# Kernel tuning notes

Measured on AMD Instinct MI355X. Metric: run time of the kernel, lower is better.

The kernel has to match this reference:

```python
import jax, jax.numpy as jnp
import numpy as np

S, L, T, E, H = 512, 5, 20, 768, 64


def setup_inputs() -> dict:
    key = jax.random.key(0)
    ks = jax.random.split(key, 32)

    def p(k, shape, scale=0.05):
        return jax.random.normal(k, shape, dtype=jnp.float32) * scale

    return {
        "text_input": jax.random.normal(ks[0], (S, L, T, E), dtype=jnp.float32),
        "time_inputs": jax.random.uniform(ks[1], (S, L, T), dtype=jnp.float32),
        # TimeLSTM per-stock params (gate order f, i, o, c_tmp)
        "Wall": p(ks[2], (S, H, 4 * H)), "bWall": p(ks[3], (S, 4 * H)),
        "Uall": p(ks[4], (S, E, 4 * H)), "bUall": p(ks[5], (S, 4 * H)),
        "Wd": p(ks[6], (S, H, H)), "bWd": p(ks[7], (S, H)),
        # shared text/day Attention per stock
        "W1": p(ks[8], (S, H, H)), "b1": p(ks[9], (S, H)),
        "W2": p(ks[10], (S, H, H)), "b2": p(ks[11], (S, H)),
        "V": p(ks[12], (S, H, 1)), "bV": p(ks[13], (S, 1)),
        # day nn.LSTM per stock (gate order i, f, g, o)
        "Wih": p(ks[14], (S, H, 4 * H)), "Whh": p(ks[15], (S, H, 4 * H)),
        "bih": p(ks[16], (S, 4 * H)), "bhh": p(ks[17], (S, 4 * H)),
        # shared output head
        "lin_w": p(ks[18], (H, 1)), "lin_b": p(ks[19], (1,)),
        "no_stocks": S,
    }


def _forward(text_input, time_inputs, Wall, bWall, Uall, bUall, Wd, bWd,
             W1, b1, W2, b2, V, bV, Wih, Whh, bih, bhh, lin_w, lin_b, no_stocks):
    def per_stock(x, ts, Wall, bWall, Uall, bUall, Wd, bWd,
                  W1, b1, W2, b2, V, bV, Wih, Whh, bih, bhh):
        # x: [L, T, E], ts: [L, T] -- lookback days are an inner batch for the TimeLSTM
        u = jnp.einsum('lte,eg->ltg', x, Uall) + bUall  # [L, T, 4H]

        def step(carry, inp):
            h, c = carry                 # [L, H]
            u_t, ts_t = inp              # [L, 4H], [L]
            c_s1 = jnp.tanh(c @ Wd + bWd)
            c_adj = (c - c_s1) + c_s1 * ts_t[:, None]
            gates = h @ Wall + bWall + u_t
            f, i, o, c_tmp = jnp.split(gates, 4, axis=1)
            f = jax.nn.sigmoid(f)
            i = jax.nn.sigmoid(i)
            o = jax.nn.sigmoid(o)
            c_tmp = jax.nn.sigmoid(c_tmp)  # sigmoid (not tanh), faithful to source
            c_new = f * c_adj + i * c_tmp
            h_new = o * jnp.tanh(c_new)
            return (h_new, c_new), o     # module collects the o gate as 'outputs'

        init = (jnp.zeros((L, H), x.dtype), jnp.zeros((L, H), x.dtype))
        (h_fin, _), o_seq = jax.lax.scan(step, init, (u.transpose(1, 0, 2), ts.T))
        full = o_seq.transpose(1, 0, 2)  # [L, T, H]

        # text attention: score = V(tanh(W1(last) + W2(full))), softmax over T
        score = jnp.tanh((h_fin @ W1 + b1)[:, None, :] + full @ W2 + b2) @ V + bV  # [L, T, 1]
        aw = jax.nn.softmax(score, axis=1)
        text_vec = jnp.sum(aw * full, axis=1)  # [L, H]

        # day nn.LSTM: input (1, L, H) seq-first => one cell step with batch=L, zero state
        h0 = jnp.zeros((L, H), x.dtype)
        g = text_vec @ Wih + bih + h0 @ Whh + bhh
        gi, gf, gg, go = jnp.split(g, 4, axis=1)
        c_d = jax.nn.sigmoid(gi) * jnp.tanh(gg)  # f * c0 = 0
        h_d = jax.nn.sigmoid(go) * jnp.tanh(c_d)  # [L, H]; output == h_n here

        # day attention reuses the SAME text_attention weights; full == last == h_d
        s2 = jnp.tanh(h_d @ W1 + b1 + h_d @ W2 + b2) @ V + bV  # [L, 1]
        aw2 = jax.nn.softmax(s2, axis=0)
        return jnp.sum(aw2 * h_d, axis=0)  # [H]

    ft_vec = jax.vmap(per_stock)(text_input, time_inputs, Wall, bWall, Uall, bUall,
                                 Wd, bWd, W1, b1, W2, b2, V, bV,
                                 Wih, Whh, bih, bhh)  # [S, H]
    return jax.nn.leaky_relu(ft_vec @ lin_w + lin_b, negative_slope=0.01)  # [S, 1]


def reference(text_input, time_inputs, Wall, bWall, Uall, bUall, Wd, bWd,
              W1, b1, W2, b2, V, bV, Wih, Whh, bih, bhh, lin_w, lin_b, no_stocks):
    return _forward(text_input, time_inputs, Wall, bWall, Uall, bUall, Wd, bWd,
                    W1, b1, W2, b2, V, bV, Wih, Whh, bih, bhh, lin_w, lin_b, no_stocks)
```

## Files before the change

kernel.cpp:

```cpp
#include <hip/hip_runtime.h>
#include <cstddef>

#define NS 512
#define NL 5
#define NT 20
#define NE 768
#define NH 64
#define NG 256

__device__ __forceinline__ float sigf(float x) { return 1.0f / (1.0f + expf(-x)); }
__device__ __forceinline__ float bcast(float v, int k) {
    return __int_as_float(__builtin_amdgcn_readlane(__float_as_int(v), k));
}

typedef __fp16 h16x2 __attribute__((ext_vector_type(2)));
typedef _Float16 f16x8 __attribute__((ext_vector_type(8)));
typedef __attribute__((ext_vector_type(4))) float f32x4;

union PkU { h16x2 h; unsigned u; };

__device__ __forceinline__ void split_pk(float a, float b, unsigned& hi, unsigned& lo) {
    PkU H, L;
    H.h = __builtin_amdgcn_cvt_pkrtz(a, b);
    float ra = a - (float)H.h[0];
    float rb = b - (float)H.h[1];
    L.h = __builtin_amdgcn_cvt_pkrtz(ra, rb);
    hi = H.u; lo = L.u;
}

__device__ __forceinline__ void stage8(const float v[8], unsigned short* base, unsigned off) {
    uint4 ph, pl;
    split_pk(v[0], v[1], ph.x, pl.x);
    split_pk(v[2], v[3], ph.y, pl.y);
    split_pk(v[4], v[5], ph.z, pl.z);
    split_pk(v[6], v[7], ph.w, pl.w);
    *(uint4*)&base[off]       = ph;
    *(uint4*)&base[off + 512] = pl;
}

__global__ __launch_bounds__(512, 4) void k_gemm_u(
    const float* __restrict__ x, const float* __restrict__ U,
    const float* __restrict__ bU, float* __restrict__ u)
{
    __shared__ unsigned short Af[8 * 2 * 512];
    __shared__ unsigned short Bf[8 * 2 * 512];
    const int bid = blockIdx.x;
    const int s = bid >> 1, half = bid & 1;
    const int tid = threadIdx.x;
    const int wave = tid >> 6, lane = tid & 63;
    const int wm = wave & 1, wn = wave >> 1;
    const float* xg = x + (size_t)s * (NL * NT * NE);
    const float* Ug = U + (size_t)s * (NE * NG) + half * 128;

    f32x4 acc[4][2] = {};

    const int arow = tid >> 2, ab = tid & 3;
    const unsigned a_off = ((unsigned)(arow >> 4) * 2) * 512 + ((arow & 15) + 16 * ab) * 8;
    const int bcol = tid & 127, bkq = tid >> 7;
    const unsigned b_off = ((unsigned)(bcol >> 4) * 2) * 512 + ((bcol & 15) + 16 * bkq) * 8;

    float av[8], bv[8];
    {
        const float* pa = xg + (size_t)arow * NE + ab * 8;
        if (arow < 100) {
            float4 q0 = *(const float4*)pa, q1 = *(const float4*)(pa + 4);
            av[0]=q0.x; av[1]=q0.y; av[2]=q0.z; av[3]=q0.w;
            av[4]=q1.x; av[5]=q1.y; av[6]=q1.z; av[7]=q1.w;
        } else {
            #pragma unroll
            for (int j = 0; j < 8; ++j) av[j] = 0.0f;
        }
        #pragma unroll
        for (int j = 0; j < 8; ++j)
            bv[j] = Ug[(size_t)(8 * bkq + j) * NG + bcol];
    }

    for (int st = 0; st < 24; ++st) {
        stage8(av, Af, a_off);
        stage8(bv, Bf, b_off);
        __syncthreads();

        if (st + 1 < 24) {
            const int k0 = (st + 1) * 32;
            const float* pa = xg + (size_t)arow * NE + k0 + ab * 8;
            if (arow < 100) {
                float4 q0 = *(const float4*)pa, q1 = *(const float4*)(pa + 4);
                av[0]=q0.x; av[1]=q0.y; av[2]=q0.z; av[3]=q0.w;
                av[4]=q1.x; av[5]=q1.y; av[6]=q1.z; av[7]=q1.w;
            } else {
                #pragma unroll
                for (int j = 0; j < 8; ++j) av[j] = 0.0f;
            }
            #pragma unroll
            for (int j = 0; j < 8; ++j)
                bv[j] = Ug[(size_t)(k0 + 8 * bkq + j) * NG + bcol];
        }

        f16x8 bh[2], bl[2];
        #pragma unroll
        for (int ni = 0; ni < 2; ++ni) {
            const unsigned nt = wn * 2 + ni;
            bh[ni] = *(const f16x8*)&Bf[(nt * 2 + 0) * 512 + lane * 8];
            bl[ni] = *(const f16x8*)&Bf[(nt * 2 + 1) * 512 + lane * 8];
        }
        #pragma unroll
        for (int mi = 0; mi < 4; ++mi) {
            const unsigned mt = wm * 4 + mi;
            f16x8 ah = *(const f16x8*)&Af[(mt * 2 + 0) * 512 + lane * 8];
            f16x8 al = *(const f16x8*)&Af[(mt * 2 + 1) * 512 + lane * 8];
            #pragma unroll
            for (int ni = 0; ni < 2; ++ni) {
                acc[mi][ni] = __builtin_amdgcn_mfma_f32_16x16x32_f16(ah, bh[ni], acc[mi][ni], 0, 0, 0);
                acc[mi][ni] = __builtin_amdgcn_mfma_f32_16x16x32_f16(ah, bl[ni], acc[mi][ni], 0, 0, 0);
                acc[mi][ni] = __builtin_amdgcn_mfma_f32_16x16x32_f16(al, bh[ni], acc[mi][ni], 0, 0, 0);
            }
        }
        __syncthreads();
    }

    const int c_sub = 4 * (lane >> 4);
    #pragma unroll
    for (int ni = 0; ni < 2; ++ni) {
        const int gcol = half * 128 + (wn * 2 + ni) * 16 + (lane & 15);
        const float bb = bU[(size_t)s * NG + gcol];
        #pragma unroll
        for (int mi = 0; mi < 4; ++mi) {
            const int grow0 = wm * 64 + mi * 16 + c_sub;
            #pragma unroll
            for (int r = 0; r < 4; ++r) {
                const int grow = grow0 + r;
                if (grow < 100) {
                    const int ld = grow / 20, td = grow % 20;
                    u[(((size_t)s * NT + td) * NL + ld) * NG + gcol] = acc[mi][ni][r] + bb;
                }
            }
        }
    }
}

#define R_WD    0
#define R_GATES 4096
#define R_HS    5376
#define R_TS    5696
#define R_TOT   5796

__global__ __launch_bounds__(320, 4) void k_recur(
    float* __restrict__ u, const float* __restrict__ ti,
    const float* __restrict__ Wall, const float* __restrict__ bWall,
    const float* __restrict__ Wd, const float* __restrict__ bWd)
{
    __shared__ float sm[R_TOT];
    const int s = blockIdx.x;
    const int tid = threadIdx.x;
    const int lq = tid >> 6, hh = tid & 63;
    const int lane = hh;
    float* ug = u + (size_t)s * NT * NL * NG;

    for (int i = tid; i < 1024; i += 320)
        *(float4*)&sm[R_WD + i * 4] = *(const float4*)(Wd + (size_t)s * 4096 + i * 4);
    if (tid < NL * NT) sm[R_TS + tid] = ti[(size_t)s * NL * NT + tid];
    sm[R_HS + tid] = 0.0f;
    const float bwd_r = bWd[(size_t)s * NH + hh];
    float c_reg = 0.0f;
    float wall_r[NH];
    float bwall_r = 0.0f, uc[NL];
    if (tid < NG) {
        bwall_r = bWall[(size_t)s * NG + tid];
        const float* wp = Wall + (size_t)s * (NH * NG) + tid;
        #pragma unroll
        for (int k = 0; k < NH; ++k) wall_r[k] = wp[(size_t)k * NG];
        #pragma unroll
        for (int l = 0; l < NL; ++l) uc[l] = ug[(size_t)l * NG + tid];
    }
    __syncthreads();

    for (int t = 0; t < NT; ++t) {
        float un[NL];
        if (tid < NG) {
            if (t + 1 < NT) {
                #pragma unroll
                for (int l = 0; l < NL; ++l)
                    un[l] = ug[(size_t)((t + 1) * NL + l) * NG + tid];
            } else {
                #pragma unroll
                for (int l = 0; l < NL; ++l) un[l] = 0.0f;
            }
            float hreg[NL];
            #pragma unroll
            for (int l = 0; l < NL; ++l) hreg[l] = sm[R_HS + l * NH + lane];
            float gv[NL];
            #pragma unroll
            for (int l = 0; l < NL; ++l) gv[l] = bwall_r + uc[l];
            #pragma unroll
            for (int k = 0; k < NH; ++k) {
                float w = wall_r[k];
                #pragma unroll
                for (int l = 0; l < NL; ++l)
                    gv[l] += bcast(hreg[l], k) * w;
            }
            #pragma unroll
            for (int l = 0; l < NL; ++l)
                sm[R_GATES + l * NG + tid] = sigf(gv[l]);
        }
        float ssum = bwd_r;
        #pragma unroll
        for (int k = 0; k < NH; ++k)
            ssum += bcast(c_reg, k) * sm[R_WD + k * NH + hh];
        float cs1 = tanhf(ssum);
        float ca = c_reg - cs1 + cs1 * sm[R_TS + lq * NT + t];
        __syncthreads();
        {
            float f  = sm[R_GATES + lq * NG + hh];
            float ii = sm[R_GATES + lq * NG + 64 + hh];
            float oo = sm[R_GATES + lq * NG + 128 + hh];
            float ct = sm[R_GATES + lq * NG + 192 + hh];
            float cn = f * ca + ii * ct;
            c_reg = cn;
            sm[R_HS + tid] = oo * tanhf(cn);
            ug[(size_t)(t * NL + lq) * NG + hh] = oo;
        }
        __syncthreads();
        if (tid < NG) {
            #pragma unroll
            for (int l = 0; l < NL; ++l) uc[l] = un[l];
        }
    }
    ug[(size_t)(0 * NL + lq) * NG + 64 + hh] = sm[R_HS + tid];
}

#define P_W1    0
#define P_W2    4096
#define P_FULLO 8192
#define P_HS    14592
#define P_TQ    14912
#define P_CA    15232
#define P_SC    15552
#define P_B0    15652
#define P_B1    15716
#define P_BVV   15780
#define P_BV1   15844
#define P_TOT   15848

__global__ __launch_bounds__(320, 2) void k_post(
    const float* __restrict__ u,
    const float* __restrict__ W1, const float* __restrict__ b1,
    const float* __restrict__ W2, const float* __restrict__ b2,
    const float* __restrict__ V, const float* __restrict__ bV,
    const float* __restrict__ Wih, const float* __restrict__ bih,
    const float* __restrict__ bhh, const float* __restrict__ lin_w,
    const float* __restrict__ lin_b, float* __restrict__ out)
{
    __shared__ float sm[P_TOT];
    const int s = blockIdx.x;
    const int tid = threadIdx.x;
    const int lq = tid >> 6, hh = tid & 63;
    const int lane = hh;
    const float* ug = u + (size_t)s * NT * NL * NG;

    for (int i = tid; i < 1024; i += 320)
        *(float4*)&sm[P_W1 + i * 4] = *(const float4*)(W1 + (size_t)s * 4096 + i * 4);
    for (int i = tid; i < 1024; i += 320)
        *(float4*)&sm[P_W2 + i * 4] = *(const float4*)(W2 + (size_t)s * 4096 + i * 4);
    for (int i = tid; i < 1600; i += 320) {
        const int idx = i >> 4;
        const int l = idx / NT, t = idx % NT;
        const int k4 = (i & 15) * 4;
        *(float4*)&sm[P_FULLO + idx * NH + k4] =
            *(const float4*)(ug + (size_t)(t * NL + l) * NG + k4);
    }
    sm[P_HS + tid] = ug[(size_t)(0 * NL + lq) * NG + 64 + hh];
    if (tid < NH) {
        sm[P_B0 + tid]  = b1[(size_t)s * NH + tid];
        sm[P_B1 + tid]  = b2[(size_t)s * NH + tid];
        sm[P_BVV + tid] = V[(size_t)s * NH + tid];
    }
    if (tid == 0) sm[P_BV1] = bV[s];
    __syncthreads();

    {
        float qv = sm[P_B0 + hh];
        for (int k4 = 0; k4 < NH; k4 += 4) {
            float4 hv = *(const float4*)&sm[P_HS + lq * NH + k4];
            qv += hv.x * sm[P_W1 + (k4 + 0) * NH + hh]
                + hv.y * sm[P_W1 + (k4 + 1) * NH + hh]
                + hv.z * sm[P_W1 + (k4 + 2) * NH + hh]
                + hv.w * sm[P_W1 + (k4 + 3) * NH + hh];
        }
        sm[P_TQ + tid] = qv;
    }
    __syncthreads();

    for (int lt = lq; lt < NL * NT; lt += 5) {
        int l = lt / NT;
        float v = sm[P_TQ + l * NH + lane] + sm[P_B1 + lane];
        for (int k4 = 0; k4 < NH; k4 += 4) {
            float4 fv = *(const float4*)&sm[P_FULLO + lt * NH + k4];
            v += fv.x * sm[P_W2 + (k4 + 0) * NH + lane]
               + fv.y * sm[P_W2 + (k4 + 1) * NH + lane]
               + fv.z * sm[P_W2 + (k4 + 2) * NH + lane]
               + fv.w * sm[P_W2 + (k4 + 3) * NH + lane];
        }
        v = tanhf(v) * sm[P_BVV + lane];
        #pragma unroll
        for (int m = 32; m > 0; m >>= 1) v += __shfl_xor(v, m, 64);
        if (lane == 0) sm[P_SC + lt] = v + sm[P_BV1];
    }
    __syncthreads();

    if (tid < NL) {
        float mx = -1e30f;
        for (int t = 0; t < NT; ++t) mx = fmaxf(mx, sm[P_SC + tid * NT + t]);
        float sum = 0.0f;
        for (int t = 0; t < NT; ++t) {
            float e = expf(sm[P_SC + tid * NT + t] - mx);
            sm[P_SC + tid * NT + t] = e;
            sum += e;
        }
        float inv = 1.0f / sum;
        for (int t = 0; t < NT; ++t) sm[P_SC + tid * NT + t] *= inv;
    }
    __syncthreads();

    {
        float sv = 0.0f;
        #pragma unroll
        for (int t = 0; t < NT; ++t)
            sv += sm[P_SC + lq * NT + t] * sm[P_FULLO + (lq * NT + t) * NH + hh];
        sm[P_CA + tid] = sv;
    }
    __syncthreads();

    if (tid < NG) {
        float bsum = bih[(size_t)s * NG + tid] + bhh[(size_t)s * NG + tid];
        float d[NL];
        #pragma unroll
        for (int l = 0; l < NL; ++l) d[l] = bsum;
        for (int k = 0; k < NH; ++k) {
            float wk = Wih[((size_t)s * NH + k) * NG + tid];
            #pragma unroll
            for (int l = 0; l < NL; ++l)
                d[l] += sm[P_CA + l * NH + k] * wk;
        }
        #pragma unroll
        for (int l = 0; l < NL; ++l)
            sm[P_FULLO + l * NG + tid] = d[l];
    }
    __syncthreads();
    {
        float gi = sm[P_FULLO + lq * NG + hh];
        float gg = sm[P_FULLO + lq * NG + 128 + hh];
        float go = sm[P_FULLO + lq * NG + 192 + hh];
        float cd = sigf(gi) * tanhf(gg);
        sm[P_TQ + tid] = sigf(go) * tanhf(cd);
    }
    __syncthreads();

    {
        float v = sm[P_B0 + lane] + sm[P_B1 + lane];
        for (int k4 = 0; k4 < NH; k4 += 4) {
            float4 hv = *(const float4*)&sm[P_TQ + lq * NH + k4];
            v += hv.x * (sm[P_W1 + (k4 + 0) * NH + lane] + sm[P_W2 + (k4 + 0) * NH + lane])
               + hv.y * (sm[P_W1 + (k4 + 1) * NH + lane] + sm[P_W2 + (k4 + 1) * NH + lane])
               + hv.z * (sm[P_W1 + (k4 + 2) * NH + lane] + sm[P_W2 + (k4 + 2) * NH + lane])
               + hv.w * (sm[P_W1 + (k4 + 3) * NH + lane] + sm[P_W2 + (k4 + 3) * NH + lane]);
        }
        v = tanhf(v) * sm[P_BVV + lane];
        #pragma unroll
        for (int m = 32; m > 0; m >>= 1) v += __shfl_xor(v, m, 64);
        if (lane == 0) sm[P_SC + lq] = v + sm[P_BV1];
    }
    __syncthreads();
    if (tid == 0) {
        float mx = -1e30f;
        for (int l = 0; l < NL; ++l) mx = fmaxf(mx, sm[P_SC + l]);
        float sum = 0.0f;
        for (int l = 0; l < NL; ++l) {
            float e = expf(sm[P_SC + l] - mx);
            sm[P_SC + l] = e;
            sum += e;
        }
        float inv = 1.0f / sum;
        for (int l = 0; l < NL; ++l) sm[P_SC + l] *= inv;
    }
    __syncthreads();

    if (tid < NH) {
        float fv = 0.0f;
        #pragma unroll
        for (int l = 0; l < NL; ++l)
            fv += sm[P_SC + l] * sm[P_TQ + l * NH + tid];
        fv *= lin_w[tid];
        #pragma unroll
        for (int m = 32; m > 0; m >>= 1) fv += __shfl_xor(fv, m, 64);
        if (tid == 0) {
            float val = fv + lin_b[0];
            out[s] = val > 0.0f ? val : 0.01f * val;
        }
    }
}

extern "C" void kernel_launch(void* const* d_in, const int* in_sizes, int n_in,
                              void* d_out, int out_size, void* d_ws, size_t ws_size,
                              hipStream_t stream) {
    (void)in_sizes; (void)n_in; (void)out_size; (void)ws_size;
    const float* x     = (const float*)d_in[0];
    const float* ti    = (const float*)d_in[1];
    const float* Wall  = (const float*)d_in[2];
    const float* bWall = (const float*)d_in[3];
    const float* Uall  = (const float*)d_in[4];
    const float* bUall = (const float*)d_in[5];
    const float* Wd    = (const float*)d_in[6];
    const float* bWd   = (const float*)d_in[7];
    const float* W1    = (const float*)d_in[8];
    const float* b1    = (const float*)d_in[9];
    const float* W2    = (const float*)d_in[10];
    const float* b2    = (const float*)d_in[11];
    const float* V     = (const float*)d_in[12];
    const float* bV    = (const float*)d_in[13];
    const float* Wih   = (const float*)d_in[14];
    const float* bih   = (const float*)d_in[16];
    const float* bhh   = (const float*)d_in[17];
    const float* lin_w = (const float*)d_in[18];
    const float* lin_b = (const float*)d_in[19];
    float* out = (float*)d_out;
    float* u = (float*)d_ws;

    k_gemm_u<<<NS * 2, 512, 0, stream>>>(x, Uall, bUall, u);
    k_recur<<<NS, 320, 0, stream>>>(u, ti, Wall, bWall, Wd, bWd);
    k_post<<<NS, 320, 0, stream>>>(u, W1, b1, W2, b2, V, bV,
                                   Wih, bih, bhh, lin_w, lin_b, out);
}
```

Before: 871.4 us.

## Move TimeLSTM recurrence matmuls to split-fp16 MFMA with register-resident weight fragments

Replaces the per-step scalar readlane-broadcast FMA loops for h@Wall and c@Wd with 16x16x32 fp16 MFMA ops. fp32 precision is approximated by a hi/lo fp16 split using three MFMAs per k-step. Weights are packed once into LDS in fragment layout and held in registers across all 20 steps. The block grows to 512 threads (8 waves), with the gate/cell update done by 320 threads. This removes a long serial scalar FMA chain per timestep, at the cost of per-step packing of h and c, wasted MFMA rows (5 of 16 used) and lower occupancy.

```diff
diff --git a/kernel.cpp b/kernel.cpp
--- a/kernel.cpp
+++ b/kernel.cpp
@@ -9,15 +9,13 @@
 #define NG 256
 
 __device__ __forceinline__ float sigf(float x) { return 1.0f / (1.0f + expf(-x)); }
-__device__ __forceinline__ float bcast(float v, int k) {
-    return __int_as_float(__builtin_amdgcn_readlane(__float_as_int(v), k));
-}
 
 typedef __fp16 h16x2 __attribute__((ext_vector_type(2)));
 typedef _Float16 f16x8 __attribute__((ext_vector_type(8)));
 typedef __attribute__((ext_vector_type(4))) float f32x4;
 
 union PkU { h16x2 h; unsigned u; };
+union FrU { uint4 u4; f16x8 h8; };
 
 __device__ __forceinline__ void split_pk(float a, float b, unsigned& hi, unsigned& lo) {
     PkU H, L;
@@ -28,12 +26,16 @@
     hi = H.u; lo = L.u;
 }
 
-__device__ __forceinline__ void stage8(const float v[8], unsigned short* base, unsigned off) {
-    uint4 ph, pl;
+__device__ __forceinline__ void pack8(const float v[8], uint4& ph, uint4& pl) {
     split_pk(v[0], v[1], ph.x, pl.x);
     split_pk(v[2], v[3], ph.y, pl.y);
     split_pk(v[4], v[5], ph.z, pl.z);
     split_pk(v[6], v[7], ph.w, pl.w);
+}
+
+__device__ __forceinline__ void stage8(const float v[8], unsigned short* base, unsigned off) {
+    uint4 ph, pl;
+    pack8(v, ph, pl);
     *(uint4*)&base[off]       = ph;
     *(uint4*)&base[off + 512] = pl;
 }
@@ -138,94 +140,180 @@
     }
 }
 
-#define R_WD    0
-#define R_GATES 4096
-#define R_HS    5376
-#define R_TS    5696
-#define R_TOT   5796
-
-__global__ __launch_bounds__(320, 4) void k_recur(
+__global__ __launch_bounds__(512, 1) void k_recur(
     float* __restrict__ u, const float* __restrict__ ti,
     const float* __restrict__ Wall, const float* __restrict__ bWall,
     const float* __restrict__ Wd, const float* __restrict__ bWd)
 {
-    __shared__ float sm[R_TOT];
+    __shared__ unsigned short WF[16 * 2 * 2 * 512];
+    __shared__ unsigned short DF[4 * 2 * 2 * 512];
+    __shared__ float GATES[NL * NG];
+    __shared__ float WDC[NL * NH];
+    __shared__ float HSP[NL * 68];
+    __shared__ float CSP[NL * 68];
+    __shared__ float TSH[NL * NT];
+
     const int s = blockIdx.x;
     const int tid = threadIdx.x;
+    const int wave = tid >> 6, lane = tid & 63;
+    float* ug = u + (size_t)s * NT * NL * NG;
+
+    {
+        const float* Wg = Wall + (size_t)s * (NH * NG);
+        const int col = tid & 255, og = tid >> 8;
+        #pragma unroll
+        for (int ks = 0; ks < 2; ++ks) {
+            #pragma unroll
+            for (int o2 = 0; o2 < 2; ++o2) {
+                const int oct = og * 2 + o2;
+                float w8[8];
+                #pragma unroll
+                for (int j = 0; j < 8; ++j)
+                    w8[j] = Wg[(size_t)(ks * 32 + oct * 8 + j) * NG + col];
+                uint4 ph, pl;
+                pack8(w8, ph, pl);
+                const unsigned base =
+                    (((unsigned)(col >> 4) * 2 + ks) * 2 + 0) * 512 + ((col & 15) + 16 * oct) * 8;
+                *(uint4*)&WF[base]       = ph;
+                *(uint4*)&WF[base + 512] = pl;
+            }
+        }
+        const float* Dg = Wd + (size_t)s * (NH * NH);
+        const int dcol = tid & 63, d8 = tid >> 6;
+        const int dks = d8 >> 2, doct = d8 & 3;
+        float w8[8];
+        #pragma unroll
+        for (int j = 0; j < 8; ++j)
+            w8[j] = Dg[(size_t)(dks * 32 + doct * 8 + j) * NH + dcol];
+        uint4 ph, pl;
+        pack8(w8, ph, pl);
+        const unsigned base =
+            (((unsigned)(dcol >> 4) * 2 + dks) * 2 + 0) * 512 + ((dcol & 15) + 16 * doct) * 8;
+        *(uint4*)&DF[base]       = ph;
+        *(uint4*)&DF[base + 512] = pl;
+    }
+    for (int i = tid; i < NL * 68; i += 512) { HSP[i] = 0.0f; CSP[i] = 0.0f; }
+    if (tid < NL * NT) TSH[tid] = ti[(size_t)s * NL * NT + tid];
+    __syncthreads();
+
+    const int nT = (wave < 4) ? 3 : 2;
+    f16x8 Bh[3][2], Bl[3][2];
+    #pragma unroll
+    for (int t2 = 0; t2 < 3; ++t2) {
+        if (t2 < nT) {
+            const int tc = wave + t2 * 8;
+            #pragma unroll
+            for (int ks = 0; ks < 2; ++ks) {
+                const unsigned short* src = (tc < 16)
+                    ? &WF[(((unsigned)tc * 2 + ks) * 2 + 0) * 512 + lane * 8]
+                    : &DF[(((unsigned)(tc - 16) * 2 + ks) * 2 + 0) * 512 + lane * 8];
+                Bh[t2][ks] = *(const f16x8*)src;
+                Bl[t2][ks] = *(const f16x8*)(src + 512);
+            }
+        }
+    }
+
     const int lq = tid >> 6, hh = tid & 63;
-    const int lane = hh;
-    float* ug = u + (size_t)s * NT * NL * NG;
-
-    for (int i = tid; i < 1024; i += 320)
-        *(float4*)&sm[R_WD + i * 4] = *(const float4*)(Wd + (size_t)s * 4096 + i * 4);
-    if (tid < NL * NT) sm[R_TS + tid] = ti[(size_t)s * NL * NT + tid];
-    sm[R_HS + tid] = 0.0f;
-    const float bwd_r = bWd[(size_t)s * NH + hh];
-    float c_reg = 0.0f;
-    float wall_r[NH];
-    float bwall_r = 0.0f, uc[NL];
-    if (tid < NG) {
-        bwall_r = bWall[(size_t)s * NG + tid];
-        const float* wp = Wall + (size_t)s * (NH * NG) + tid;
-        #pragma unroll
-        for (int k = 0; k < NH; ++k) wall_r[k] = wp[(size_t)k * NG];
-        #pragma unroll
-        for (int l = 0; l < NL; ++l) uc[l] = ug[(size_t)l * NG + tid];
-    }
-    __syncthreads();
-
+    float bw[4], bwd_r = 0.0f, un[4], c_reg = 0.0f, h_reg = 0.0f;
+    if (tid < 320) {
+        #pragma unroll
+        for (int j = 0; j < 4; ++j) {
+            bw[j] = bWall[(size_t)s * NG + j * 64 + hh];
+            un[j] = ug[(size_t)(0 * NL + lq) * NG + j * 64 + hh];
+        }
+        bwd_r = bWd[(size_t)s * NH + hh];
+    }
+
+    const int arow = lane & 15, akq = lane >> 4;
     for (int t = 0; t < NT; ++t) {
-        float un[NL];
-        if (tid < NG) {
-            if (t + 1 < NT) {
-                #pragma unroll
-                for (int l = 0; l < NL; ++l)
-                    un[l] = ug[(size_t)((t + 1) * NL + l) * NG + tid];
+        f16x8 ah[2], al[2], cah[2], cal[2];
+        #pragma unroll
+        for (int ks = 0; ks < 2; ++ks) {
+            float v[8];
+            if (arow < NL) {
+                float4 q0 = *(const float4*)&HSP[arow * 68 + ks * 32 + akq * 8];
+                float4 q1 = *(const float4*)&HSP[arow * 68 + ks * 32 + akq * 8 + 4];
+                v[0]=q0.x; v[1]=q0.y; v[2]=q0.z; v[3]=q0.w;
+                v[4]=q1.x; v[5]=q1.y; v[6]=q1.z; v[7]=q1.w;
             } else {
                 #pragma unroll
-                for (int l = 0; l < NL; ++l) un[l] = 0.0f;
-            }
-            float hreg[NL];
-            #pragma unroll
-            for (int l = 0; l < NL; ++l) hreg[l] = sm[R_HS + l * NH + lane];
-            float gv[NL];
-            #pragma unroll
-            for (int l = 0; l < NL; ++l) gv[l] = bwall_r + uc[l];
-            #pragma unroll
-            for (int k = 0; k < NH; ++k) {
-                float w = wall_r[k];
+                for (int j = 0; j < 8; ++j) v[j] = 0.0f;
+            }
+            FrU H, L;
+            pack8(v, H.u4, L.u4);
+            ah[ks] = H.h8; al[ks] = L.h8;
+        }
+        if (wave < 4) {
+            #pragma unroll
+            for (int ks = 0; ks < 2; ++ks) {
+                float v[8];
+                if (arow < NL) {
+                    float4 q0 = *(const float4*)&CSP[arow * 68 + ks * 32 + akq * 8];
+                    float4 q1 = *(const float4*)&CSP[arow * 68 + ks * 32 + akq * 8 + 4];
+                    v[0]=q0.x; v[1]=q0.y; v[2]=q0.z; v[3]=q0.w;
+                    v[4]=q1.x; v[5]=q1.y; v[6]=q1.z; v[7]=q1.w;
+                } else {
+                    #pragma unroll
+                    for (int j = 0; j < 8; ++j) v[j] = 0.0f;
+                }
+                FrU H, L;
+                pack8(v, H.u4, L.u4);
+                cah[ks] = H.h8; cal[ks] = L.h8;
+            }
+        }
+        #pragma unroll
+        for (int t2 = 0; t2 < 3; ++t2) {
+            if (t2 < nT) {
+                const int tc = wave + t2 * 8;
+                const bool isWd = (tc >= 16);
+                f32x4 acc = {};
                 #pragma unroll
-                for (int l = 0; l < NL; ++l)
-                    gv[l] += bcast(hreg[l], k) * w;
-            }
-            #pragma unroll
-            for (int l = 0; l < NL; ++l)
-                sm[R_GATES + l * NG + tid] = sigf(gv[l]);
-        }
-        float ssum = bwd_r;
-        #pragma unroll
-        for (int k = 0; k < NH; ++k)
-            ssum += bcast(c_reg, k) * sm[R_WD + k * NH + hh];
-        float cs1 = tanhf(ssum);
-        float ca = c_reg - cs1 + cs1 * sm[R_TS + lq * NT + t];
+                for (int ks = 0; ks < 2; ++ks) {
+                    f16x8 A_h = isWd ? cah[ks] : ah[ks];
+                    f16x8 A_l = isWd ? cal[ks] : al[ks];
+                    acc = __builtin_amdgcn_mfma_f32_16x16x32_f16(A_h, Bh[t2][ks], acc, 0, 0, 0);
+                    acc = __builtin_amdgcn_mfma_f32_16x16x32_f16(A_h, Bl[t2][ks], acc, 0, 0, 0);
+                    acc = __builtin_amdgcn_mfma_f32_16x16x32_f16(A_l, Bh[t2][ks], acc, 0, 0, 0);
+                }
+                #pragma unroll
+                for (int r = 0; r < 4; ++r) {
+                    const int row = 4 * akq + r;
+                    if (row < NL) {
+                        if (!isWd) GATES[row * NG + tc * 16 + arow] = acc[r];
+                        else       WDC[row * NH + (tc - 16) * 16 + arow] = acc[r];
+                    }
+                }
+            }
+        }
+        float unx[4];
+        if (tid < 320 && t + 1 < NT) {
+            #pragma unroll
+            for (int j = 0; j < 4; ++j)
+                unx[j] = ug[(size_t)((t + 1) * NL + lq) * NG + j * 64 + hh];
+        }
         __syncthreads();
-        {
-            float f  = sm[R_GATES + lq * NG + hh];
-            float ii = sm[R_GATES + lq * NG + 64 + hh];
-            float oo = sm[R_GATES + lq * NG + 128 + hh];
-            float ct = sm[R_GATES + lq * NG + 192 + hh];
-            float cn = f * ca + ii * ct;
+
+        if (tid < 320) {
+            float g0 = GATES[lq * NG + hh]        + bw[0] + un[0];
+            float g1 = GATES[lq * NG + 64 + hh]   + bw[1] + un[1];
+            float g2 = GATES[lq * NG + 128 + hh]  + bw[2] + un[2];
+            float g3 = GATES[lq * NG + 192 + hh]  + bw[3] + un[3];
+            float f  = sigf(g0), ii = sigf(g1), oo = sigf(g2), ct = sigf(g3);
+            float cs1 = tanhf(WDC[lq * NH + hh] + bwd_r);
+            float ca  = c_reg - cs1 + cs1 * TSH[lq * NT + t];
+            float cn  = f * ca + ii * ct;
             c_reg = cn;
-            sm[R_HS + tid] = oo * tanhf(cn);
+            h_reg = oo * tanhf(cn);
+            HSP[lq * 68 + hh] = h_reg;
+            CSP[lq * 68 + hh] = cn;
             ug[(size_t)(t * NL + lq) * NG + hh] = oo;
+            #pragma unroll
+            for (int j = 0; j < 4; ++j) un[j] = unx[j];
         }
         __syncthreads();
-        if (tid < NG) {
-            #pragma unroll
-            for (int l = 0; l < NL; ++l) uc[l] = un[l];
-        }
-    }
-    ug[(size_t)(0 * NL + lq) * NG + 64 + hh] = sm[R_HS + tid];
+    }
+    if (tid < 320)
+        ug[(size_t)(0 * NL + lq) * NG + 64 + hh] = h_reg;
 }
 
 #define P_W1    0
@@ -426,7 +514,7 @@
     float* u = (float*)d_ws;
 
     k_gemm_u<<<NS * 2, 512, 0, stream>>>(x, Uall, bUall, u);
-    k_recur<<<NS, 320, 0, stream>>>(u, ti, Wall, bWall, Wd, bWd);
+    k_recur<<<NS, 512, 0, stream>>>(u, ti, Wall, bWall, Wd, bWd);
     k_post<<<NS, 320, 0, stream>>>(u, W1, b1, W2, b2, V, bV,
                                    Wih, bih, bhh, lin_w, lin_b, out);
 }
```

After: 859.4 us. About the same (-1.4%).
